# Kernel tuning notes

Measured on AMD Instinct MI355X. Metric: run time of the kernel, lower is better.

## Reference

```python
import jax, jax.numpy as jnp
import numpy as np

SPS_AMPLIFY = 1.5
SPS_DAMPEN = 0.3
SPS_DEEP_QUESTION = 0.1
SPS_EXCLAIM = 0.85
SPS_QUESTION = 0.25
SPS_SUPER_EXCLAIM = 0.95

B, S, D = 4, 2048, 1024
NUM_HEADS = 16
HEAD_DIM = D // NUM_HEADS
SCALE = HEAD_DIM ** (-0.5)


def sps_pro(x):
    """Piecewise elementwise modulation based on sigmoid(x) bands."""
    xn = jax.nn.sigmoid(x)
    # bands: xn>0.95 -> 2.0 ; 0.85<xn<=0.95 -> 1.5 ; xn<0.1 -> 0.1 ;
    #        0.1<=xn<0.25 -> 0.3 ; else -> 1.0
    mult = jnp.where(
        xn > SPS_SUPER_EXCLAIM, 2.0,
        jnp.where(xn > SPS_EXCLAIM, SPS_AMPLIFY,
                  jnp.where(xn < SPS_DEEP_QUESTION, 0.1,
                            jnp.where(xn < SPS_QUESTION, SPS_DAMPEN, 1.0))))
    return x * mult


def setup_inputs() -> dict:
    key = jax.random.key(0)
    k0, k1, k2, k3, k4 = jax.random.split(key, 5)
    s = 1.0 / np.sqrt(D)
    return {
        "x": jax.random.normal(k0, (B, S, D), dtype=jnp.float32),
        "W_qkv": jax.random.uniform(k1, (D, 3 * D), dtype=jnp.float32, minval=-s, maxval=s),
        "b_qkv": jax.random.uniform(k2, (3 * D,), dtype=jnp.float32, minval=-s, maxval=s),
        "W_proj": jax.random.uniform(k3, (D, D), dtype=jnp.float32, minval=-s, maxval=s),
        "b_proj": jax.random.uniform(k4, (D,), dtype=jnp.float32, minval=-s, maxval=s),
    }


def reference(x, W_qkv, b_qkv, W_proj, b_proj):
    qkv = jnp.einsum('bsd,de->bse', x, W_qkv) + b_qkv  # [B,S,3D]
    q, k, v = jnp.split(qkv, 3, axis=-1)               # each [B,S,D]
    attn = jnp.einsum('bsd,btd->bst', q, k) * SCALE    # [B,S,S]
    attn = sps_pro(attn)
    attn = jax.nn.softmax(attn, axis=-1)
    out = jnp.einsum('bst,btd->bsd', attn, v)          # [B,S,D]
    out = jnp.einsum('bsd,de->bse', out, W_proj) + b_proj
    return out
```

## Files before the change

### kernel.cpp

```cpp
#include <hip/hip_runtime.h>
#include <hip/hip_bf16.h>
#include <hip/hip_fp16.h>
#include <stdint.h>

typedef __attribute__((ext_vector_type(8))) _Float16 f16x8;
typedef __attribute__((ext_vector_type(4))) float f32x4;

__device__ __forceinline__ void async16(void* lds, const void* g) {
  __builtin_amdgcn_global_load_lds(
      (const __attribute__((address_space(1))) void*)g,
      (__attribute__((address_space(3))) void*)lds, 16, 0, 0);
}

__device__ __forceinline__ uint16_t f2h_u(float f) {
  union { __half h; uint16_t u; } c;
  c.h = __float2half(f);
  return c.u;
}

__global__ __launch_bounds__(256)
void conv_f2h(const float* __restrict__ in, uint16_t* __restrict__ out, int n4) {
  int i = blockIdx.x * 256 + threadIdx.x;
  if (i >= n4) return;
  float4 v = ((const float4*)in)[i];
  ushort4 o;
  o.x = f2h_u(v.x); o.y = f2h_u(v.y); o.z = f2h_u(v.z); o.w = f2h_u(v.w);
  ((ushort4*)out)[i] = o;
}

__global__ __launch_bounds__(256)
void trans_f2h(const float* __restrict__ in, uint16_t* __restrict__ out,
               int ldin, int ldout) {
  __shared__ float t[64][65];
  const int tx = threadIdx.x & 63, ty = threadIdx.x >> 6;
  const int r0 = blockIdx.y * 64, c0 = blockIdx.x * 64;
#pragma unroll
  for (int i = 0; i < 16; ++i)
    t[ty + i * 4][tx] = in[(size_t)(r0 + ty + i * 4) * ldin + c0 + tx];
  __syncthreads();
#pragma unroll
  for (int i = 0; i < 16; ++i)
    out[(size_t)(c0 + ty + i * 4) * ldout + r0 + tx] = f2h_u(t[tx][ty + i * 4]);
}

template <int EPI>
__global__ __launch_bounds__(512, 2)
void gemm256(const uint16_t* __restrict__ A, const uint16_t* __restrict__ B,
             void* __restrict__ Cv, void* __restrict__ Cv2, void* __restrict__ Cv3,
             const float* __restrict__ bias,
             int nT, int lda, int ldb, int ldc,
             long long strA, long long strB, long long strC) {
  extern __shared__ uint16_t lds_u16[];

  const int gx = gridDim.x, gy = gridDim.y;
  const int nwg = gx * gy * gridDim.z;
  const int fid = blockIdx.x + gx * (blockIdx.y + gy * blockIdx.z);
  const int fs = (fid & 7) * (nwg >> 3) + (fid >> 3);
  const int bx = fs % gx;
  const int by = (fs / gx) % gy;
  const int bz = fs / (gx * gy);

  const int tid = threadIdx.x;
  const int l = tid & 63;
  const int w = tid >> 6;
  const int wm = w >> 1, wn = w & 1;
  const int l15 = l & 15, l4 = l >> 4;
  const int rowBase = bx * 256, colBase = by * 128;
  const uint16_t* Ag = A + (size_t)bz * strA;
  const uint16_t* Bg = B + (size_t)bz * strB;

  const uint16_t* pA[4];
  const uint16_t* pB[2];
#pragma unroll
  for (int u = 0; u < 4; ++u) {
    int c = tid + (u << 9);
    int cs = c ^ ((c >> 3) & 7);
    pA[u] = Ag + (size_t)(rowBase + (cs >> 3)) * lda + (cs & 7) * 8;
  }
#pragma unroll
  for (int u = 0; u < 2; ++u) {
    int c = tid + (u << 9);
    int cs = c ^ ((c >> 3) & 7);
    pB[u] = Bg + (size_t)(colBase + (cs >> 3)) * ldb + (cs & 7) * 8;
  }

  f32x4 acc[4][4];
#pragma unroll
  for (int m = 0; m < 4; ++m)
#pragma unroll
    for (int n = 0; n < 4; ++n)
      acc[m][n] = (f32x4){0.f, 0.f, 0.f, 0.f};

#define STAGE_H(t2, s2, h)                                                     \
  {                                                                            \
    const int kb_ = (t2) << 6;                                                 \
    uint16_t* dA_ = lds_u16 + (s2) * 24576;                                    \
    uint16_t* dB_ = dA_ + 16384;                                               \
    async16(&dA_[(size_t)(tid + ((2 * (h)) << 9)) * 8], pA[2 * (h)] + kb_);    \
    async16(&dA_[(size_t)(tid + ((2 * (h) + 1) << 9)) * 8], pA[2 * (h) + 1] + kb_); \
    async16(&dB_[(size_t)(tid + ((h) << 9)) * 8], pB[h] + kb_);                \
  }

  STAGE_H(0, 0, 0) STAGE_H(0, 0, 1)
  STAGE_H(1, 1, 0) STAGE_H(1, 1, 1)
  asm volatile("s_waitcnt vmcnt(6)" ::: "memory");
  __builtin_amdgcn_s_barrier();

  int sl = 0;
  for (int t = 0; t < nT; ++t) {
    int s2 = sl + 2; if (s2 >= 3) s2 -= 3;
    const uint16_t* As = lds_u16 + sl * 24576;
    const uint16_t* Bs = As + 16384;
#pragma unroll
    for (int ks = 0; ks < 2; ++ks) {
      f16x8 af[4], bf[4];
#pragma unroll
      for (int m = 0; m < 4; ++m) {
        const int r = wm * 64 + m * 16 + l15;
        const int byt = r * 128 + ((ks * 64 + l4 * 16) ^ ((r & 7) << 4));
        af[m] = *(const f16x8*)((const char*)As + byt);
      }
#pragma unroll
      for (int n = 0; n < 4; ++n) {
        const int r = wn * 64 + n * 16 + l15;
        const int byt = r * 128 + ((ks * 64 + l4 * 16) ^ ((r & 7) << 4));
        bf[n] = *(const f16x8*)((const char*)Bs + byt);
      }
      if (t + 2 < nT) STAGE_H(t + 2, s2, ks)
      __builtin_amdgcn_s_barrier();
      __builtin_amdgcn_s_setprio(1);
#pragma unroll
      for (int m = 0; m < 4; ++m)
#pragma unroll
        for (int n = 0; n < 4; ++n)
          acc[m][n] = __builtin_amdgcn_mfma_f32_16x16x32_f16(af[m], bf[n], acc[m][n], 0, 0, 0);
      __builtin_amdgcn_s_setprio(0);
      if (ks == 0) {
        __builtin_amdgcn_s_barrier();
      } else if (t + 1 < nT) {
        if (t + 2 < nT) {
          asm volatile("s_waitcnt vmcnt(6)" ::: "memory");
        } else {
          asm volatile("s_waitcnt vmcnt(0)" ::: "memory");
        }
        __builtin_amdgcn_s_barrier();
      }
    }
    sl = (sl == 2) ? 0 : sl + 1;
  }
#undef STAGE_H

  const int orow0 = rowBase + wm * 64 + l4 * 4;
  const int ocol0 = colBase + wn * 64 + l15;
  if (EPI == 0) {
    uint16_t* qd = (uint16_t*)Cv;
    uint16_t* kd = (uint16_t*)Cv2;
    uint16_t* vt = (uint16_t*)Cv3;
#pragma unroll
    for (int n = 0; n < 4; ++n) {
      const int gcol = ocol0 + n * 16;
      const float bv = bias[gcol];
      if (gcol < 2048) {
        uint16_t* base = (gcol < 1024 ? qd : kd) + (gcol & 1023);
#pragma unroll
        for (int m = 0; m < 4; ++m)
#pragma unroll
          for (int j = 0; j < 4; ++j) {
            const int grow = orow0 + m * 16 + j;
            base[(size_t)(grow >> 11) * 2097152 + (size_t)(grow & 2047) * 1024] =
                f2h_u(acc[m][n][j] + bv);
          }
      } else {
        const int d = gcol - 2048;
#pragma unroll
        for (int m = 0; m < 4; ++m) {
          const int grow0 = orow0 + m * 16;
          ushort4 o;
          o.x = f2h_u(acc[m][n][0] + bv);
          o.y = f2h_u(acc[m][n][1] + bv);
          o.z = f2h_u(acc[m][n][2] + bv);
          o.w = f2h_u(acc[m][n][3] + bv);
          *(ushort4*)&vt[(size_t)(grow0 >> 11) * 2097152 + (size_t)d * 2048 +
                         (grow0 & 2047)] = o;
        }
      }
    }
  } else if (EPI == 1) {
    uint16_t* C = (uint16_t*)Cv + (size_t)bz * strC;
#pragma unroll
    for (int n = 0; n < 4; ++n)
#pragma unroll
      for (int m = 0; m < 4; ++m)
#pragma unroll
        for (int j = 0; j < 4; ++j) {
          float xs = acc[m][n][j] * 0.125f;
          float mult = (xs > 2.94443897916644f) ? 2.0f
                     : (xs > 1.73460105538811f) ? 1.5f
                     : (xs < -2.19722457733622f) ? 0.1f
                     : (xs < -1.09861228866811f) ? 0.3f
                                                 : 1.0f;
          C[(size_t)(orow0 + m * 16 + j) * ldc + ocol0 + n * 16] = f2h_u(xs * mult);
        }
  } else if (EPI == 3) {
    uint16_t* C = (uint16_t*)Cv + (size_t)bz * strC;
#pragma unroll
    for (int n = 0; n < 4; ++n)
#pragma unroll
      for (int m = 0; m < 4; ++m)
#pragma unroll
        for (int j = 0; j < 4; ++j)
          C[(size_t)(orow0 + m * 16 + j) * ldc + ocol0 + n * 16] = f2h_u(acc[m][n][j]);
  } else {
    float* C = (float*)Cv;
#pragma unroll
    for (int n = 0; n < 4; ++n) {
      const float bv = bias[ocol0 + n * 16];
#pragma unroll
      for (int m = 0; m < 4; ++m)
#pragma unroll
        for (int j = 0; j < 4; ++j)
          C[(size_t)(orow0 + m * 16 + j) * ldc + ocol0 + n * 16] = acc[m][n][j] + bv;
    }
  }
}

__global__ __launch_bounds__(256)
void softmax_rows(uint16_t* __restrict__ P) {
  const size_t row = blockIdx.x;
  uint16_t* p = P + row * 2048;
  const int tid = threadIdx.x;
  uint4 raw = *(const uint4*)(p + tid * 8);
  uint32_t w[4] = {raw.x, raw.y, raw.z, raw.w};
  float v[8];
#pragma unroll
  for (int q = 0; q < 4; ++q) {
    __half2 h = *(__half2*)&w[q];
    float2 f = __half22float2(h);
    v[2 * q] = f.x;
    v[2 * q + 1] = f.y;
  }
  float mx = v[0];
#pragma unroll
  for (int j = 1; j < 8; ++j) mx = fmaxf(mx, v[j]);
#pragma unroll
  for (int o = 32; o > 0; o >>= 1) mx = fmaxf(mx, __shfl_xor(mx, o));
  __shared__ float redm[4], reds[4];
  if ((tid & 63) == 0) redm[tid >> 6] = mx;
  __syncthreads();
  mx = fmaxf(fmaxf(redm[0], redm[1]), fmaxf(redm[2], redm[3]));
  float e[8];
  float se = 0.f;
#pragma unroll
  for (int j = 0; j < 8; ++j) { e[j] = __expf(v[j] - mx); se += e[j]; }
#pragma unroll
  for (int o = 32; o > 0; o >>= 1) se += __shfl_xor(se, o);
  if ((tid & 63) == 0) reds[tid >> 6] = se;
  __syncthreads();
  se = (reds[0] + reds[1]) + (reds[2] + reds[3]);
  const float inv = 1.0f / se;
  uint32_t wo[4];
#pragma unroll
  for (int q = 0; q < 4; ++q) {
    uint16_t a = f2h_u(e[2 * q] * inv);
    uint16_t b = f2h_u(e[2 * q + 1] * inv);
    wo[q] = (uint32_t)a | ((uint32_t)b << 16);
  }
  uint4 ov;
  ov.x = wo[0]; ov.y = wo[1]; ov.z = wo[2]; ov.w = wo[3];
  *(uint4*)(p + tid * 8) = ov;
}

extern "C" void kernel_launch(void* const* d_in, const int* in_sizes, int n_in,
                              void* d_out, int out_size, void* d_ws, size_t ws_size,
                              hipStream_t stream) {
  const float* x     = (const float*)d_in[0];
  const float* Wqkv  = (const float*)d_in[1];
  const float* bqkv  = (const float*)d_in[2];
  const float* Wproj = (const float*)d_in[3];
  const float* bproj = (const float*)d_in[4];
  float* out = (float*)d_out;

  char* ws = (char*)d_ws;
  size_t off = 0;
  auto alloc = [&](size_t bytes) -> void* {
    void* p = ws + off;
    off += (bytes + 255) & ~(size_t)255;
    return p;
  };
  uint16_t* xh    = (uint16_t*)alloc(8192ULL * 1024 * 2);
  uint16_t* WqkvT = (uint16_t*)alloc(3072ULL * 1024 * 2);
  uint16_t* WpT   = (uint16_t*)alloc(1024ULL * 1024 * 2);
  uint16_t* qh    = (uint16_t*)alloc(4ULL * 2048 * 1024 * 2);
  uint16_t* kh    = (uint16_t*)alloc(4ULL * 2048 * 1024 * 2);
  uint16_t* vT    = (uint16_t*)alloc(4ULL * 1024 * 2048 * 2);
  uint16_t* Pm    = (uint16_t*)alloc(4ULL * 2048 * 2048 * 2);
  uint16_t* ao    = xh;

  conv_f2h<<<8192, 256, 0, stream>>>(x, xh, 2097152);
  trans_f2h<<<dim3(48, 16), 256, 0, stream>>>(Wqkv, WqkvT, 3072, 1024);
  trans_f2h<<<dim3(16, 16), 256, 0, stream>>>(Wproj, WpT, 1024, 1024);
  gemm256<0><<<dim3(32, 24, 1), 512, 147456, stream>>>(
      xh, WqkvT, qh, kh, vT, bqkv, 16, 1024, 1024, 0, 0, 0, 0);
  gemm256<1><<<dim3(8, 16, 4), 512, 147456, stream>>>(
      qh, kh, Pm, nullptr, nullptr, nullptr, 16, 1024, 1024, 2048,
      2097152LL, 2097152LL, 4194304LL);
  softmax_rows<<<8192, 256, 0, stream>>>(Pm);
  gemm256<3><<<dim3(8, 8, 4), 512, 147456, stream>>>(
      Pm, vT, ao, nullptr, nullptr, nullptr, 32, 2048, 2048, 1024,
      4194304LL, 2097152LL, 2097152LL);
  gemm256<4><<<dim3(32, 8, 1), 512, 147456, stream>>>(
      ao, WpT, out, nullptr, nullptr, bproj, 16, 1024, 1024, 1024, 0, 0, 0);
}
```

Before: 235.4 us.

## Add 256x256-tile GEMM kernel for QKV and QK^T, reorder staging in small GEMM

Adds a new gemm_big kernel with a 256x256 output tile per workgroup. It uses 8 waves in a 2x4 layout, double-buffered LDS, and a four-phase MFMA schedule that reuses A and B fragments across quadrants. The QKV projection and the QK^T score GEMM switch to it, which halves their grid sizes and raises arithmetic intensity per LDS load. The remaining small-tile kernel now issues the next stage's async loads at the top of each K iteration and drops the per-half-step barriers, leaving one barrier per iteration. The trade-off is higher register pressure from 32 accumulators per thread, fewer workgroups to fill the CUs, and possible LDS hazards from the relaxed barriers.

```diff
diff --git a/kernel.cpp b/kernel.cpp
--- a/kernel.cpp
+++ b/kernel.cpp
@@ -45,9 +45,209 @@
 
 template <int EPI>
 __global__ __launch_bounds__(512, 2)
-void gemm256(const uint16_t* __restrict__ A, const uint16_t* __restrict__ B,
-             void* __restrict__ Cv, void* __restrict__ Cv2, void* __restrict__ Cv3,
-             const float* __restrict__ bias,
+void gemm_big(const uint16_t* __restrict__ A, const uint16_t* __restrict__ B,
+              void* __restrict__ Cv, void* __restrict__ Cv2, void* __restrict__ Cv3,
+              const float* __restrict__ bias,
+              int nT, int lda, int ldb, int ldc,
+              long long strA, long long strB, long long strC) {
+  extern __shared__ uint16_t lds_u16[];
+
+  const int gx = gridDim.x, gy = gridDim.y;
+  const int nwg = gx * gy * gridDim.z;
+  const int fid = blockIdx.x + gx * (blockIdx.y + gy * blockIdx.z);
+  const int fs = (fid & 7) * (nwg >> 3) + (fid >> 3);
+  const int bx = fs % gx;
+  const int by = (fs / gx) % gy;
+  const int bz = fs / (gx * gy);
+
+  const int tid = threadIdx.x;
+  const int l = tid & 63;
+  const int w = tid >> 6;
+  const int wm = w >> 2, wn = w & 3;
+  const int l15 = l & 15, l4 = l >> 4;
+  const int rowBase = bx * 256, colBase = by * 256;
+  const uint16_t* Ag = A + (size_t)bz * strA;
+  const uint16_t* Bg = B + (size_t)bz * strB;
+
+  const uint16_t* pA[4];
+  const uint16_t* pB[4];
+#pragma unroll
+  for (int u = 0; u < 4; ++u) {
+    int c = tid + (u << 9);
+    int cs = c ^ ((c >> 3) & 7);
+    pA[u] = Ag + (size_t)(rowBase + (cs >> 3)) * lda + (cs & 7) * 8;
+    pB[u] = Bg + (size_t)(colBase + (cs >> 3)) * ldb + (cs & 7) * 8;
+  }
+
+  f32x4 acc[8][4];
+#pragma unroll
+  for (int m = 0; m < 8; ++m)
+#pragma unroll
+    for (int n = 0; n < 4; ++n)
+      acc[m][n] = (f32x4){0.f, 0.f, 0.f, 0.f};
+
+#define STAGE(t2, s2)                                                          \
+  {                                                                            \
+    const int kb_ = (t2) << 6;                                                 \
+    uint16_t* dA_ = lds_u16 + (s2) * 32768;                                    \
+    uint16_t* dB_ = dA_ + 16384;                                               \
+    _Pragma("unroll") for (int u = 0; u < 4; ++u) {                            \
+      async16(&dA_[(size_t)(tid + (u << 9)) * 8], pA[u] + kb_);                \
+      async16(&dB_[(size_t)(tid + (u << 9)) * 8], pB[u] + kb_);                \
+    }                                                                          \
+  }
+
+#define ABYTE(r, ks) ((r) * 128 + ((((ks) * 64) + l4 * 16) ^ (((r) & 7) << 4)))
+
+  STAGE(0, 0)
+  STAGE(1, 1)
+  asm volatile("s_waitcnt vmcnt(8)" ::: "memory");
+  __builtin_amdgcn_s_barrier();
+
+  for (int t = 0; t < nT; ++t) {
+    const int sl = t & 1;
+    const uint16_t* As = lds_u16 + sl * 32768;
+    const uint16_t* Bs = As + 16384;
+    f16x8 a0[4][2], a1[4][2], b0[2][2], b1[2][2];
+#pragma unroll
+    for (int mr = 0; mr < 4; ++mr) {
+      const int r = wm * 128 + mr * 16 + l15;
+#pragma unroll
+      for (int ks = 0; ks < 2; ++ks)
+        a0[mr][ks] = *(const f16x8*)((const char*)As + ABYTE(r, ks));
+    }
+#pragma unroll
+    for (int nr = 0; nr < 2; ++nr) {
+      const int r = wn * 64 + nr * 16 + l15;
+#pragma unroll
+      for (int ks = 0; ks < 2; ++ks)
+        b0[nr][ks] = *(const f16x8*)((const char*)Bs + ABYTE(r, ks));
+    }
+    __builtin_amdgcn_s_setprio(1);
+#pragma unroll
+    for (int ks = 0; ks < 2; ++ks)
+#pragma unroll
+      for (int mr = 0; mr < 4; ++mr)
+#pragma unroll
+        for (int nr = 0; nr < 2; ++nr)
+          acc[mr][nr] = __builtin_amdgcn_mfma_f32_16x16x32_f16(a0[mr][ks], b0[nr][ks], acc[mr][nr], 0, 0, 0);
+    __builtin_amdgcn_s_setprio(0);
+    __builtin_amdgcn_s_barrier();
+#pragma unroll
+    for (int nr = 0; nr < 2; ++nr) {
+      const int r = wn * 64 + 32 + nr * 16 + l15;
+#pragma unroll
+      for (int ks = 0; ks < 2; ++ks)
+        b1[nr][ks] = *(const f16x8*)((const char*)Bs + ABYTE(r, ks));
+    }
+    __builtin_amdgcn_s_setprio(1);
+#pragma unroll
+    for (int ks = 0; ks < 2; ++ks)
+#pragma unroll
+      for (int mr = 0; mr < 4; ++mr)
+#pragma unroll
+        for (int nr = 0; nr < 2; ++nr)
+          acc[mr][2 + nr] = __builtin_amdgcn_mfma_f32_16x16x32_f16(a0[mr][ks], b1[nr][ks], acc[mr][2 + nr], 0, 0, 0);
+    __builtin_amdgcn_s_setprio(0);
+    __builtin_amdgcn_s_barrier();
+#pragma unroll
+    for (int mr = 0; mr < 4; ++mr) {
+      const int r = wm * 128 + 64 + mr * 16 + l15;
+#pragma unroll
+      for (int ks = 0; ks < 2; ++ks)
+        a1[mr][ks] = *(const f16x8*)((const char*)As + ABYTE(r, ks));
+    }
+    __builtin_amdgcn_s_setprio(1);
+#pragma unroll
+    for (int ks = 0; ks < 2; ++ks)
+#pragma unroll
+      for (int mr = 0; mr < 4; ++mr)
+#pragma unroll
+        for (int nr = 0; nr < 2; ++nr)
+          acc[4 + mr][2 + nr] = __builtin_amdgcn_mfma_f32_16x16x32_f16(a1[mr][ks], b1[nr][ks], acc[4 + mr][2 + nr], 0, 0, 0);
+    __builtin_amdgcn_s_setprio(0);
+    __builtin_amdgcn_s_barrier();
+    if (t + 2 < nT) STAGE(t + 2, sl)
+    __builtin_amdgcn_s_setprio(1);
+#pragma unroll
+    for (int ks = 0; ks < 2; ++ks)
+#pragma unroll
+      for (int mr = 0; mr < 4; ++mr)
+#pragma unroll
+        for (int nr = 0; nr < 2; ++nr)
+          acc[4 + mr][nr] = __builtin_amdgcn_mfma_f32_16x16x32_f16(a1[mr][ks], b0[nr][ks], acc[4 + mr][nr], 0, 0, 0);
+    __builtin_amdgcn_s_setprio(0);
+    if (t + 1 < nT) {
+      if (t + 2 < nT) {
+        asm volatile("s_waitcnt vmcnt(8)" ::: "memory");
+      } else {
+        asm volatile("s_waitcnt vmcnt(0)" ::: "memory");
+      }
+      __builtin_amdgcn_s_barrier();
+    }
+  }
+#undef STAGE
+#undef ABYTE
+
+  if (EPI == 0) {
+    uint16_t* qd = (uint16_t*)Cv;
+    uint16_t* kd = (uint16_t*)Cv2;
+    uint16_t* vt = (uint16_t*)Cv3;
+#pragma unroll
+    for (int ni = 0; ni < 4; ++ni) {
+      const int gcol = colBase + wn * 64 + ni * 16 + l15;
+      const float bv = bias[gcol];
+      if (gcol < 2048) {
+        uint16_t* base = (gcol < 1024 ? qd : kd) + (gcol & 1023);
+#pragma unroll
+        for (int mi = 0; mi < 8; ++mi)
+#pragma unroll
+          for (int j = 0; j < 4; ++j) {
+            const int grow = rowBase + wm * 128 + mi * 16 + l4 * 4 + j;
+            base[(size_t)(grow >> 11) * 2097152 + (size_t)(grow & 2047) * 1024] =
+                f2h_u(acc[mi][ni][j] + bv);
+          }
+      } else {
+        const int d = gcol - 2048;
+#pragma unroll
+        for (int mi = 0; mi < 8; ++mi) {
+          const int grow0 = rowBase + wm * 128 + mi * 16 + l4 * 4;
+          ushort4 o;
+          o.x = f2h_u(acc[mi][ni][0] + bv);
+          o.y = f2h_u(acc[mi][ni][1] + bv);
+          o.z = f2h_u(acc[mi][ni][2] + bv);
+          o.w = f2h_u(acc[mi][ni][3] + bv);
+          *(ushort4*)&vt[(size_t)(grow0 >> 11) * 2097152 + (size_t)d * 2048 +
+                         (grow0 & 2047)] = o;
+        }
+      }
+    }
+  } else {
+    uint16_t* C = (uint16_t*)Cv + (size_t)bz * strC;
+#pragma unroll
+    for (int ni = 0; ni < 4; ++ni) {
+      const int gcol = colBase + wn * 64 + ni * 16 + l15;
+#pragma unroll
+      for (int mi = 0; mi < 8; ++mi)
+#pragma unroll
+        for (int j = 0; j < 4; ++j) {
+          const int grow = rowBase + wm * 128 + mi * 16 + l4 * 4 + j;
+          float xs = acc[mi][ni][j] * 0.125f;
+          float mult = (xs > 2.94443897916644f) ? 2.0f
+                     : (xs > 1.73460105538811f) ? 1.5f
+                     : (xs < -2.19722457733622f) ? 0.1f
+                     : (xs < -1.09861228866811f) ? 0.3f
+                                                 : 1.0f;
+          C[(size_t)grow * ldc + gcol] = f2h_u(xs * mult);
+        }
+    }
+  }
+}
+
+template <int EPI>
+__global__ __launch_bounds__(512, 2)
+void gemm_sm(const uint16_t* __restrict__ A, const uint16_t* __restrict__ B,
+             void* __restrict__ Cv, const float* __restrict__ bias,
              int nT, int lda, int ldb, int ldc,
              long long strA, long long strB, long long strC) {
   extern __shared__ uint16_t lds_u16[];
@@ -91,24 +291,26 @@
     for (int n = 0; n < 4; ++n)
       acc[m][n] = (f32x4){0.f, 0.f, 0.f, 0.f};
 
-#define STAGE_H(t2, s2, h)                                                     \
+#define STAGE(t2, s2)                                                          \
   {                                                                            \
     const int kb_ = (t2) << 6;                                                 \
     uint16_t* dA_ = lds_u16 + (s2) * 24576;                                    \
     uint16_t* dB_ = dA_ + 16384;                                               \
-    async16(&dA_[(size_t)(tid + ((2 * (h)) << 9)) * 8], pA[2 * (h)] + kb_);    \
-    async16(&dA_[(size_t)(tid + ((2 * (h) + 1) << 9)) * 8], pA[2 * (h) + 1] + kb_); \
-    async16(&dB_[(size_t)(tid + ((h) << 9)) * 8], pB[h] + kb_);                \
-  }
-
-  STAGE_H(0, 0, 0) STAGE_H(0, 0, 1)
-  STAGE_H(1, 1, 0) STAGE_H(1, 1, 1)
+    _Pragma("unroll") for (int u = 0; u < 4; ++u)                              \
+        async16(&dA_[(size_t)(tid + (u << 9)) * 8], pA[u] + kb_);              \
+    _Pragma("unroll") for (int u = 0; u < 2; ++u)                              \
+        async16(&dB_[(size_t)(tid + (u << 9)) * 8], pB[u] + kb_);              \
+  }
+
+  STAGE(0, 0)
+  STAGE(1, 1)
   asm volatile("s_waitcnt vmcnt(6)" ::: "memory");
   __builtin_amdgcn_s_barrier();
 
   int sl = 0;
   for (int t = 0; t < nT; ++t) {
     int s2 = sl + 2; if (s2 >= 3) s2 -= 3;
+    if (t + 2 < nT) STAGE(t + 2, s2)
     const uint16_t* As = lds_u16 + sl * 24576;
     const uint16_t* Bs = As + 16384;
 #pragma unroll
@@ -126,8 +328,6 @@
         const int byt = r * 128 + ((ks * 64 + l4 * 16) ^ ((r & 7) << 4));
         bf[n] = *(const f16x8*)((const char*)Bs + byt);
       }
-      if (t + 2 < nT) STAGE_H(t + 2, s2, ks)
-      __builtin_amdgcn_s_barrier();
       __builtin_amdgcn_s_setprio(1);
 #pragma unroll
       for (int m = 0; m < 4; ++m)
@@ -135,73 +335,22 @@
         for (int n = 0; n < 4; ++n)
           acc[m][n] = __builtin_amdgcn_mfma_f32_16x16x32_f16(af[m], bf[n], acc[m][n], 0, 0, 0);
       __builtin_amdgcn_s_setprio(0);
-      if (ks == 0) {
-        __builtin_amdgcn_s_barrier();
-      } else if (t + 1 < nT) {
-        if (t + 2 < nT) {
-          asm volatile("s_waitcnt vmcnt(6)" ::: "memory");
-        } else {
-          asm volatile("s_waitcnt vmcnt(0)" ::: "memory");
-        }
-        __builtin_amdgcn_s_barrier();
+    }
+    if (t + 1 < nT) {
+      if (t + 2 < nT) {
+        asm volatile("s_waitcnt vmcnt(6)" ::: "memory");
+      } else {
+        asm volatile("s_waitcnt vmcnt(0)" ::: "memory");
       }
+      __builtin_amdgcn_s_barrier();
     }
     sl = (sl == 2) ? 0 : sl + 1;
   }
-#undef STAGE_H
+#undef STAGE
 
   const int orow0 = rowBase + wm * 64 + l4 * 4;
   const int ocol0 = colBase + wn * 64 + l15;
-  if (EPI == 0) {
-    uint16_t* qd = (uint16_t*)Cv;
-    uint16_t* kd = (uint16_t*)Cv2;
-    uint16_t* vt = (uint16_t*)Cv3;
-#pragma unroll
-    for (int n = 0; n < 4; ++n) {
-      const int gcol = ocol0 + n * 16;
-      const float bv = bias[gcol];
-      if (gcol < 2048) {
-        uint16_t* base = (gcol < 1024 ? qd : kd) + (gcol & 1023);
-#pragma unroll
-        for (int m = 0; m < 4; ++m)
-#pragma unroll
-          for (int j = 0; j < 4; ++j) {
-            const int grow = orow0 + m * 16 + j;
-            base[(size_t)(grow >> 11) * 2097152 + (size_t)(grow & 2047) * 1024] =
-                f2h_u(acc[m][n][j] + bv);
-          }
-      } else {
-        const int d = gcol - 2048;
-#pragma unroll
-        for (int m = 0; m < 4; ++m) {
-          const int grow0 = orow0 + m * 16;
-          ushort4 o;
-          o.x = f2h_u(acc[m][n][0] + bv);
-          o.y = f2h_u(acc[m][n][1] + bv);
-          o.z = f2h_u(acc[m][n][2] + bv);
-          o.w = f2h_u(acc[m][n][3] + bv);
-          *(ushort4*)&vt[(size_t)(grow0 >> 11) * 2097152 + (size_t)d * 2048 +
-                         (grow0 & 2047)] = o;
-        }
-      }
-    }
-  } else if (EPI == 1) {
-    uint16_t* C = (uint16_t*)Cv + (size_t)bz * strC;
-#pragma unroll
-    for (int n = 0; n < 4; ++n)
-#pragma unroll
-      for (int m = 0; m < 4; ++m)
-#pragma unroll
-        for (int j = 0; j < 4; ++j) {
-          float xs = acc[m][n][j] * 0.125f;
-          float mult = (xs > 2.94443897916644f) ? 2.0f
-                     : (xs > 1.73460105538811f) ? 1.5f
-                     : (xs < -2.19722457733622f) ? 0.1f
-                     : (xs < -1.09861228866811f) ? 0.3f
-                                                 : 1.0f;
-          C[(size_t)(orow0 + m * 16 + j) * ldc + ocol0 + n * 16] = f2h_u(xs * mult);
-        }
-  } else if (EPI == 3) {
+  if (EPI == 3) {
     uint16_t* C = (uint16_t*)Cv + (size_t)bz * strC;
 #pragma unroll
     for (int n = 0; n < 4; ++n)
@@ -299,15 +448,15 @@
   conv_f2h<<<8192, 256, 0, stream>>>(x, xh, 2097152);
   trans_f2h<<<dim3(48, 16), 256, 0, stream>>>(Wqkv, WqkvT, 3072, 1024);
   trans_f2h<<<dim3(16, 16), 256, 0, stream>>>(Wproj, WpT, 1024, 1024);
-  gemm256<0><<<dim3(32, 24, 1), 512, 147456, stream>>>(
+  gemm_big<0><<<dim3(32, 12, 1), 512, 131072, stream>>>(
       xh, WqkvT, qh, kh, vT, bqkv, 16, 1024, 1024, 0, 0, 0, 0);
-  gemm256<1><<<dim3(8, 16, 4), 512, 147456, stream>>>(
+  gemm_big<1><<<dim3(8, 8, 4), 512, 131072, stream>>>(
       qh, kh, Pm, nullptr, nullptr, nullptr, 16, 1024, 1024, 2048,
       2097152LL, 2097152LL, 4194304LL);
   softmax_rows<<<8192, 256, 0, stream>>>(Pm);
-  gemm256<3><<<dim3(8, 8, 4), 512, 147456, stream>>>(
-      Pm, vT, ao, nullptr, nullptr, nullptr, 32, 2048, 2048, 1024,
+  gemm_sm<3><<<dim3(8, 8, 4), 512, 147456, stream>>>(
+      Pm, vT, ao, nullptr, 32, 2048, 2048, 1024,
       4194304LL, 2097152LL, 2097152LL);
-  gemm256<4><<<dim3(32, 8, 1), 512, 147456, stream>>>(
-      ao, WpT, out, nullptr, nullptr, bproj, 16, 1024, 1024, 1024, 0, 0, 0);
-}
+  gemm_sm<4><<<dim3(32, 8, 1), 512, 147456, stream>>>(
+      ao, WpT, out, bproj, 16, 1024, 1024, 1024, 0, 0, 0);
+}
```

After: 222.9 us. 1.06x faster.
